# Performance work log

Measured on AMD Instinct MI355X. Metric: run time of the kernel, lower is better.

## Reference

```python
import jax, jax.numpy as jnp
import numpy as np

N_NODES = 50000
N_EDGES = 500000
NUM_FEAT = 128
NUM_CLASSES = 112
HID = 18
HEADS = 8
OUT_DIM = 144  # hidden_dim * heads = 18*8 = 144, also final GAT out_dim
N_GRAPHS = 64
EPS = 1e-5
NEG_SLOPE = 0.2


def setup_inputs() -> dict:
    key = jax.random.key(0)
    ks = jax.random.split(key, 32)
    f32 = jnp.float32
    def rn(k, shape, scale=0.1):
        return jax.random.normal(k, shape, f32) * scale
    x = jax.random.normal(ks[0], (N_NODES, NUM_FEAT), f32)
    edge_index = jax.random.randint(ks[1], (2, N_EDGES), 0, N_NODES)
    batch = jnp.sort(jax.random.randint(ks[2], (N_NODES,), 0, N_GRAPHS))
    D = HID * HEADS  # 144
    params = dict(
        x=x, edge_index=edge_index, batch=batch,
        We=rn(ks[3], (NUM_FEAT, D)), be=jnp.zeros((D,), f32),
        Wg=rn(ks[4], (3, D, D)),
        a_sg=rn(ks[5], (3, HEADS, HID)), a_dg=rn(ks[6], (3, HEADS, HID)),
        bg=jnp.zeros((3, D), f32),
        gam=jnp.ones((3, D), f32), bet=jnp.zeros((3, D), f32),
        W3=rn(ks[7], (D, OUT_DIM)),
        a_s3=rn(ks[8], (1, OUT_DIM)), a_d3=rn(ks[9], (1, OUT_DIM)),
        b3=jnp.zeros((OUT_DIM,), f32),
        gam3=jnp.ones((OUT_DIM,), f32), bet3=jnp.zeros((OUT_DIM,), f32),
        M1=rn(ks[10], (OUT_DIM, 72)), bm1=jnp.zeros((72,), f32),
        gm1=jnp.ones((72,), f32), bb1=jnp.zeros((72,), f32),
        M2=rn(ks[11], (72, 36)), bm2=jnp.zeros((36,), f32),
        gm2=jnp.ones((36,), f32), bb2=jnp.zeros((36,), f32),
        M3=rn(ks[12], (36, NUM_CLASSES)), bm3=jnp.zeros((NUM_CLASSES,), f32),
    )
    return params


def _gat_layer(h, src, dst, W, a_s, a_d, b, heads, out_ch):
    # PyG GATConv: per-head linear, additive attention, segment softmax over dst
    N = h.shape[0]
    hp = (h @ W).reshape(N, heads, out_ch)                 # [N,H,C]
    al_s = (hp * a_s).sum(-1)                              # [N,H]
    al_d = (hp * a_d).sum(-1)                              # [N,H]
    e = jax.nn.leaky_relu(al_s[src] + al_d[dst], NEG_SLOPE)  # [E,H]
    m = jax.ops.segment_max(e, dst, num_segments=N)
    ex = jnp.exp(e - m[dst])
    den = jax.ops.segment_sum(ex, dst, num_segments=N)
    alpha = ex / (den[dst] + 1e-16)                        # [E,H]
    out = jax.ops.segment_sum(hp[src] * alpha[..., None], dst, num_segments=N)
    return out.reshape(N, heads * out_ch) + b


def _bn(x, g, b):
    mu = x.mean(0)
    v = jnp.var(x, axis=0)
    return g * (x - mu) * jax.lax.rsqrt(v + EPS) + b


def reference(x, edge_index, batch, We, be, Wg, a_sg, a_dg, bg, gam, bet,
              W3, a_s3, a_d3, b3, gam3, bet3,
              M1, bm1, gm1, bb1, M2, bm2, gm2, bb2, M3, bm3):
    N = x.shape[0]
    loops = jnp.arange(N)  # GATConv add_self_loops=True
    src = jnp.concatenate([edge_index[0], loops])
    dst = jnp.concatenate([edge_index[1], loops])
    out = x @ We + be
    for i in range(3):
        out = _gat_layer(out, src, dst, Wg[i], a_sg[i], a_dg[i], bg[i], HEADS, HID)
        out = jax.nn.relu(out)
        out = _bn(out, gam[i], bet[i])
    out = _gat_layer(out, src, dst, W3, a_s3, a_d3, b3, 1, OUT_DIM)
    out = jax.nn.relu(out)
    out = _bn(out, gam3, bet3)
    # global mean pool over graphs
    sums = jax.ops.segment_sum(out, batch, num_segments=N_GRAPHS)
    cnt = jax.ops.segment_sum(jnp.ones((N, 1), out.dtype), batch, num_segments=N_GRAPHS)
    g = sums / jnp.maximum(cnt, 1.0)
    # PyG MLP: lin -> batchnorm -> relu (plain last layer)
    h = jax.nn.relu(_bn(g @ M1 + bm1, gm1, bb1))
    h = jax.nn.relu(_bn(h @ M2 + bm2, gm2, bb2))
    return h @ M3 + bm3
```

## Files before the change

### kernel.cpp

```cpp
#include <hip/hip_runtime.h>
#include <cstdint>

#define N_NODESC 50000
#define N_EDGESC 500000
#define E_TOT    550000
#define DIM      144
#define NGRAPH   64
#define EPSV     1e-5f
#define SCAN_NB  ((N_NODESC + 511)/512)

typedef __attribute__((ext_vector_type(8))) short bf16x8;
typedef __attribute__((ext_vector_type(4))) float f32x4;

__device__ __forceinline__ float lrelu(float x){ return x > 0.f ? x : 0.2f*x; }

__device__ __forceinline__ unsigned short f2bf(float f){
  unsigned u = __float_as_uint(f);
  u += 0x7FFF + ((u >> 16) & 1);
  return (unsigned short)(u >> 16);
}
__device__ __forceinline__ float bf2f(unsigned short b){
  return __uint_as_float(((unsigned)b) << 16);
}

__global__ void k_count(const int* __restrict__ ei, int* __restrict__ deg){
  int e = blockIdx.x*blockDim.x + threadIdx.x;
  if (e >= E_TOT) return;
  int d = (e < N_EDGESC) ? ei[N_EDGESC + e] : (e - N_EDGESC);
  atomicAdd(&deg[d], 1);
}

__global__ __launch_bounds__(256) void k_scan1(const int* __restrict__ deg,
    int* __restrict__ scanned, int* __restrict__ bsum){
  __shared__ int ls[256];
  int b = blockIdx.x, t = threadIdx.x;
  int i0 = b*512 + 2*t;
  int e0 = (i0   < N_NODESC) ? deg[i0]   : 0;
  int e1 = (i0+1 < N_NODESC) ? deg[i0+1] : 0;
  int s = e0 + e1;
  ls[t] = s;
  __syncthreads();
  #pragma unroll
  for (int ofs=1; ofs<256; ofs<<=1){
    int v = (t >= ofs) ? ls[t-ofs] : 0;
    __syncthreads();
    ls[t] += v;
    __syncthreads();
  }
  int excl = ls[t] - s;
  if (i0   < N_NODESC) scanned[i0]   = excl;
  if (i0+1 < N_NODESC) scanned[i0+1] = excl + e0;
  if (t == 255) bsum[b] = ls[255];
}

__global__ void k_scan2(int* __restrict__ bsum){
  __shared__ int ls[128];
  int t = threadIdx.x;
  int v = (t < SCAN_NB) ? bsum[t] : 0;
  ls[t] = v;
  __syncthreads();
  #pragma unroll
  for (int ofs=1; ofs<128; ofs<<=1){
    int u = (t >= ofs) ? ls[t-ofs] : 0;
    __syncthreads();
    ls[t] += u;
    __syncthreads();
  }
  if (t < SCAN_NB) bsum[t] = ls[t] - v;
}

__global__ __launch_bounds__(256) void k_scan3(const int* __restrict__ scanned,
    const int* __restrict__ bsum, int* __restrict__ row_ptr, int* __restrict__ cursor){
  int i = blockIdx.x*blockDim.x + threadIdx.x;
  if (i < N_NODESC){
    int v = scanned[i] + bsum[i >> 9];
    row_ptr[i] = v; cursor[i] = v;
  }
  if (i == 0) row_ptr[N_NODESC] = E_TOT;
}

__global__ void k_scatter(const int* __restrict__ ei, int* __restrict__ cursor,
                          int* __restrict__ col){
  int e = blockIdx.x*blockDim.x + threadIdx.x;
  if (e >= E_TOT) return;
  int s, d;
  if (e < N_EDGESC){ s = ei[e]; d = ei[N_EDGESC + e]; } else { s = e - N_EDGESC; d = s; }
  int pos = atomicAdd(&cursor[d], 1);
  col[pos] = s;
}

__global__ void k_cast(const float* __restrict__ x, unsigned short* __restrict__ xb){
  int i = blockIdx.x*blockDim.x + threadIdx.x;
  if (i < N_NODESC*128) xb[i] = f2bf(x[i]);
}

__global__ __launch_bounds__(192) void k_prep_w(
    const float* __restrict__ W, const float* __restrict__ bias_in,
    const float* __restrict__ a_s, const float* __restrict__ a_d,
    const float* __restrict__ bnsum, const float* __restrict__ bngam,
    const float* __restrict__ bnbet,
    unsigned short* __restrict__ Wt, float* __restrict__ bias2,
    int K, int SK, int H){
  __shared__ float red[256];
  int np = blockIdx.x, k = threadIdx.x;
  float sc = 1.f, sh = 0.f;
  if (k < K && bnsum){
    float mu  = bnsum[k] * (1.f/N_NODESC);
    float var = bnsum[K+k] * (1.f/N_NODESC) - mu*mu;
    float inv = rsqrtf(var + EPSV);
    sc = inv * bngam[k];
    sh = bnbet[k] - mu*sc;
  }
  float wcomb = 0.f;
  if (k < K){
    if (np < 144) wcomb = W[(size_t)k*144 + np];
    else if (H > 0){
      int c = np - 144;
      bool iss = c < 8;
      int h = iss ? c : c - 8;
      if (h < H){
        const float* av = iss ? a_s : a_d;
        int C = 144 / H;
        for (int j=0;j<C;++j) wcomb += W[(size_t)k*144 + h*C + j] * av[h*C + j];
      }
    }
  }
  if (k < SK) Wt[(size_t)np*SK + k] = f2bf(wcomb*sc);
  red[k] = (k < K) ? sh*wcomb : 0.f;
  if (k < 64) red[k+192] = 0.f;
  __syncthreads();
  #pragma unroll
  for (int s=128; s>0; s>>=1){
    if (k < s) red[k] += red[k+s];
    __syncthreads();
  }
  if (k == 0){
    float b = red[0];
    if (np < 144 && bias_in) b += bias_in[np];
    bias2[np] = b;
  }
}

template<int NT, int KS, int SK>
__global__ __launch_bounds__(256) void k_mfma_gemm(
    const unsigned short* __restrict__ A,
    const unsigned short* __restrict__ Wt,
    const float* __restrict__ bias2,
    unsigned short* __restrict__ hp,
    float* __restrict__ al_s, float* __restrict__ al_d,
    int KA, int H){
  int t = threadIdx.x;
  int wave = t >> 6, lane = t & 63;
  int c = lane & 15, quad = lane >> 4;
  int m_base = blockIdx.x*64 + wave*16;
  int mA = m_base + c; if (mA > N_NODESC-1) mA = N_NODESC-1;
  f32x4 acc[NT];
  #pragma unroll
  for (int i=0;i<NT;++i) acc[i] = (f32x4){0.f,0.f,0.f,0.f};
  const unsigned short* Arow = A + (size_t)mA*KA + quad*8;
  #pragma unroll
  for (int ks=0; ks<KS; ++ks){
    bf16x8 af = *(const bf16x8*)(Arow + ks*32);
    #pragma unroll
    for (int tt=0; tt<NT; ++tt){
      bf16x8 bfr = *(const bf16x8*)(Wt + (size_t)(tt*16 + c)*SK + ks*32 + quad*8);
      acc[tt] = __builtin_amdgcn_mfma_f32_16x16x32_bf16(af, bfr, acc[tt], 0, 0, 0);
    }
  }
  #pragma unroll
  for (int tt=0; tt<NT; ++tt){
    int n = tt*16 + c;
    float b = bias2[n];
    #pragma unroll
    for (int r=0;r<4;++r){
      int m = m_base + quad*4 + r;
      if (m < N_NODESC){
        float v = acc[tt][r] + b;
        if (n < 144){
          hp[(size_t)m*144 + n] = f2bf(v);
        } else {
          int cc = n - 144;
          if (cc < 8){ if (cc < H) al_s[m*H + cc] = v; }
          else { int h = cc - 8; if (h < H) al_d[m*H + h] = v; }
        }
      }
    }
  }
}

#define EB 8
__global__ __launch_bounds__(256) void k_edge_softmax(
    const float* __restrict__ al_s, const float* __restrict__ al_d,
    const int* __restrict__ row_ptr, const int* __restrict__ col,
    float* __restrict__ esc, int H){
  int idx = blockIdx.x*blockDim.x + threadIdx.x;
  if (idx >= N_NODESC*H) return;
  int n = idx / H, h = idx - n*H;
  int p0 = row_ptr[n], p1 = row_ptr[n+1];
  float ald = al_d[idx];
  float m = -3.4e38f;
  for (int base = p0; base < p1; base += EB){
    int cnt = min(EB, p1 - base);
    int ss[EB];
    #pragma unroll
    for (int i=0;i<EB;++i) if (i<cnt) ss[i] = col[base+i];
    float sc[EB];
    #pragma unroll
    for (int i=0;i<EB;++i) if (i<cnt) sc[i] = lrelu(al_s[ss[i]*H + h] + ald);
    #pragma unroll
    for (int i=0;i<EB;++i) if (i<cnt){
      esc[(size_t)(base+i)*H + h] = sc[i];
      m = fmaxf(m, sc[i]);
    }
  }
  float den = 0.f;
  for (int e = p0; e < p1; ++e) den += __expf(esc[(size_t)e*H + h] - m);
  float inv = 1.f/(den + 1e-16f);
  for (int e = p0; e < p1; ++e)
    esc[(size_t)e*H + h] = __expf(esc[(size_t)e*H + h] - m) * inv;
}

__global__ __launch_bounds__(256) void k_aggregate2(
    const unsigned* __restrict__ hp2, const float* __restrict__ w,
    const int* __restrict__ row_ptr, const int* __restrict__ col,
    const float* __restrict__ bias, unsigned* __restrict__ out,
    int H, int C2){
  int idx = blockIdx.x*blockDim.x + threadIdx.x;
  if (idx >= N_NODESC*72) return;
  int n = idx / 72, cp = idx - n*72;
  int h = cp / C2;
  int p0 = row_ptr[n], p1 = row_ptr[n+1];
  float a0 = 0.f, a1 = 0.f;
  for (int base = p0; base < p1; base += EB){
    int cnt = min(EB, p1 - base);
    int ss[EB]; float ww[EB];
    #pragma unroll
    for (int i=0;i<EB;++i) if (i<cnt){
      ss[i] = col[base+i];
      ww[i] = w[(size_t)(base+i)*H + h];
    }
    unsigned vv[EB];
    #pragma unroll
    for (int i=0;i<EB;++i) if (i<cnt) vv[i] = hp2[(size_t)ss[i]*72 + cp];
    #pragma unroll
    for (int i=0;i<EB;++i) if (i<cnt){
      a0 = fmaf(ww[i], __uint_as_float(vv[i] << 16), a0);
      a1 = fmaf(ww[i], __uint_as_float(vv[i] & 0xFFFF0000u), a1);
    }
  }
  int c0 = 2*cp;
  float r0 = fmaxf(a0 + bias[c0],   0.f);
  float r1 = fmaxf(a1 + bias[c0+1], 0.f);
  out[(size_t)n*72 + cp] = (unsigned)f2bf(r0) | ((unsigned)f2bf(r1) << 16);
}

#define BNS_GRID 512
__global__ __launch_bounds__(256) void k_bnstats1(const uint2* __restrict__ h4,
                                                  float* __restrict__ partials){
  __shared__ float red[252*8];
  int t = threadIdx.x;
  int r = t / 36, c = t - r*36;
  bool active = (t < 252);
  int rows = (N_NODESC + BNS_GRID - 1)/BNS_GRID;
  int n0 = blockIdx.x*rows, n1 = min(N_NODESC, n0+rows);
  float s[4] = {0,0,0,0}, q[4] = {0,0,0,0};
  if (active){
    for (int n = n0 + r; n < n1; n += 7){
      uint2 v = h4[(size_t)n*36 + c];
      float f0 = __uint_as_float(v.x << 16);
      float f1 = __uint_as_float(v.x & 0xFFFF0000u);
      float f2 = __uint_as_float(v.y << 16);
      float f3 = __uint_as_float(v.y & 0xFFFF0000u);
      s[0]+=f0; q[0]+=f0*f0; s[1]+=f1; q[1]+=f1*f1;
      s[2]+=f2; q[2]+=f2*f2; s[3]+=f3; q[3]+=f3*f3;
    }
    #pragma unroll
    for (int j=0;j<4;++j){
      red[(c*7+r)*8 + j]     = s[j];
      red[(c*7+r)*8 + 4 + j] = q[j];
    }
  }
  __syncthreads();
  if (t < 36){
    float ss[4]={0,0,0,0}, qq[4]={0,0,0,0};
    for (int rr=0; rr<7; ++rr){
      #pragma unroll
      for (int j=0;j<4;++j){
        ss[j] += red[(t*7+rr)*8 + j];
        qq[j] += red[(t*7+rr)*8 + 4 + j];
      }
    }
    float* p = partials + (size_t)blockIdx.x*288;
    #pragma unroll
    for (int j=0;j<4;++j){
      p[4*t+j]       = ss[j];
      p[144+4*t+j]   = qq[j];
    }
  }
}

__global__ __launch_bounds__(64) void k_bnstats2(const float* __restrict__ partials,
                                                 float* __restrict__ sums){
  int i = blockIdx.x, t = threadIdx.x;
  float s = 0.f;
  for (int b = t; b < BNS_GRID; b += 64) s += partials[(size_t)b*288 + i];
  #pragma unroll
  for (int o=32; o>0; o>>=1) s += __shfl_xor(s, o, 64);
  if (t == 0) sums[i] = s;
}

__device__ int lbound(const int* a, int n, int v){
  int lo = 0, hi = n;
  while (lo < hi){ int m = (lo+hi) >> 1; if (a[m] < v) lo = m+1; else hi = m; }
  return lo;
}

__global__ __launch_bounds__(128) void k_pool(const unsigned* __restrict__ h2,
    const int* __restrict__ batch, float* __restrict__ sums, int* __restrict__ cnts){
  int g = blockIdx.x & 63, part = blockIdx.x >> 6;
  __shared__ int sb[2];
  if (threadIdx.x == 0){ sb[0] = lbound(batch, N_NODESC, g); sb[1] = lbound(batch, N_NODESC, g+1); }
  __syncthreads();
  int lo = sb[0], hi = sb[1];
  int t = threadIdx.x;
  if (t < 72){
    float a0 = 0.f, a1 = 0.f;
    for (int n = lo + part; n < hi; n += 32){
      unsigned v = h2[(size_t)n*72 + t];
      a0 += __uint_as_float(v << 16);
      a1 += __uint_as_float(v & 0xFFFF0000u);
    }
    atomicAdd(&sums[g*DIM + 2*t],   a0);
    atomicAdd(&sums[g*DIM + 2*t+1], a1);
  }
  if (t == 0 && part == 0) cnts[g] = hi - lo;
}

__global__ __launch_bounds__(64) void k_mlp1(const float* __restrict__ psum,
    const int* __restrict__ cnts,
    const float* __restrict__ bn3, const float* __restrict__ gam3,
    const float* __restrict__ bet3,
    const float* __restrict__ M1, const float* __restrict__ bm1,
    const float* __restrict__ gm1, const float* __restrict__ bb1,
    float* __restrict__ h1){
  __shared__ float sSc[144], sSh[144];
  int t = threadIdx.x, c = blockIdx.x;
  for (int i=t; i<144; i+=64){
    float mu  = bn3[i] * (1.f/N_NODESC);
    float var = bn3[144+i] * (1.f/N_NODESC) - mu*mu;
    float sc  = rsqrtf(var + EPSV) * gam3[i];
    sSc[i] = sc; sSh[i] = bet3[i] - mu*sc;
  }
  __syncthreads();
  float invc = 1.f / (float)max(cnts[t], 1);
  float acc = bm1[c];
  const float* pr = psum + t*144;
  for (int k=0; k<144; ++k){
    float g = fmaf(pr[k]*invc, sSc[k], sSh[k]);
    acc = fmaf(g, M1[k*72 + c], acc);
  }
  float s = acc, q = acc*acc;
  #pragma unroll
  for (int o=32; o>0; o>>=1){ s += __shfl_xor(s, o, 64); q += __shfl_xor(q, o, 64); }
  float mu = s*(1.f/64.f), var = q*(1.f/64.f) - mu*mu;
  float v = (acc - mu)*rsqrtf(var + EPSV)*gm1[c] + bb1[c];
  h1[t*72 + c] = fmaxf(v, 0.f);
}

__global__ __launch_bounds__(64) void k_mlp2(const float* __restrict__ h1,
    const float* __restrict__ M2, const float* __restrict__ bm2,
    const float* __restrict__ gm2, const float* __restrict__ bb2,
    float* __restrict__ h2){
  int t = threadIdx.x, c = blockIdx.x;
  float acc = bm2[c];
  const float* pr = h1 + t*72;
  for (int k=0; k<72; ++k) acc = fmaf(pr[k], M2[k*36 + c], acc);
  float s = acc, q = acc*acc;
  #pragma unroll
  for (int o=32; o>0; o>>=1){ s += __shfl_xor(s, o, 64); q += __shfl_xor(q, o, 64); }
  float mu = s*(1.f/64.f), var = q*(1.f/64.f) - mu*mu;
  float v = (acc - mu)*rsqrtf(var + EPSV)*gm2[c] + bb2[c];
  h2[t*36 + c] = fmaxf(v, 0.f);
}

__global__ __launch_bounds__(64) void k_mlp3(const float* __restrict__ h2,
    const float* __restrict__ M3, const float* __restrict__ bm3,
    float* __restrict__ out){
  int t = threadIdx.x, c = blockIdx.x;
  float acc = bm3[c];
  const float* pr = h2 + t*36;
  for (int k=0; k<36; ++k) acc = fmaf(pr[k], M3[k*112 + c], acc);
  out[t*112 + c] = acc;
}

extern "C" void kernel_launch(void* const* d_in, const int* in_sizes, int n_in,
                              void* d_out, int out_size, void* d_ws, size_t ws_size,
                              hipStream_t stream){
  const float* x    = (const float*)d_in[0];
  const int*   ei   = (const int*)d_in[1];
  const int*   batch= (const int*)d_in[2];
  const float* We   = (const float*)d_in[3];
  const float* be   = (const float*)d_in[4];
  const float* Wg   = (const float*)d_in[5];
  const float* a_sg = (const float*)d_in[6];
  const float* a_dg = (const float*)d_in[7];
  const float* bg   = (const float*)d_in[8];
  const float* gam  = (const float*)d_in[9];
  const float* bet  = (const float*)d_in[10];
  const float* W3   = (const float*)d_in[11];
  const float* a_s3 = (const float*)d_in[12];
  const float* a_d3 = (const float*)d_in[13];
  const float* b3   = (const float*)d_in[14];
  const float* gam3 = (const float*)d_in[15];
  const float* bet3 = (const float*)d_in[16];
  const float* M1   = (const float*)d_in[17];
  const float* bm1  = (const float*)d_in[18];
  const float* gm1  = (const float*)d_in[19];
  const float* bb1  = (const float*)d_in[20];
  const float* M2   = (const float*)d_in[21];
  const float* bm2  = (const float*)d_in[22];
  const float* gm2  = (const float*)d_in[23];
  const float* bb2  = (const float*)d_in[24];
  const float* M3   = (const float*)d_in[25];
  const float* bm3  = (const float*)d_in[26];
  float* out = (float*)d_out;

  char* ws = (char*)d_ws;
  size_t off = 0;
  auto alloc = [&](size_t bytes)->char*{
    char* p = ws + off; off += (bytes + 255) & ~(size_t)255; return p;
  };
  unsigned short* hAb = (unsigned short*)alloc((size_t)N_NODESC*DIM*2);
  unsigned short* hp  = (unsigned short*)alloc((size_t)N_NODESC*DIM*2);
  unsigned short* xb  = (unsigned short*)alloc((size_t)N_NODESC*128*2);
  float* al_s   = (float*)alloc((size_t)N_NODESC*8*4);
  float* al_d   = (float*)alloc((size_t)N_NODESC*8*4);
  float* esc    = (float*)alloc((size_t)E_TOT*8*4);
  int* row_ptr  = (int*)alloc((size_t)(N_NODESC+1)*4);
  int* deg      = (int*)alloc((size_t)N_NODESC*4);
  int* cursor   = (int*)alloc((size_t)N_NODESC*4);
  int* scanned  = (int*)alloc((size_t)N_NODESC*4);
  int* bsum     = (int*)alloc((size_t)SCAN_NB*4);
  int* col      = (int*)alloc((size_t)E_TOT*4);
  float* bns4   = (float*)alloc(4*2*DIM*4);
  float* partials = (float*)alloc((size_t)BNS_GRID*288*4);
  float* psum   = (float*)alloc((size_t)NGRAPH*DIM*4);
  int* pcnt     = (int*)alloc(NGRAPH*4);
  float* h1buf  = (float*)alloc((size_t)NGRAPH*72*4);
  float* h2buf  = (float*)alloc((size_t)NGRAPH*36*4);
  unsigned short* Wt = (unsigned short*)alloc((size_t)160*168*2);
  float* bias2  = (float*)alloc(160*4);
  (void)ws_size; (void)n_in; (void)in_sizes; (void)out_size;

  const int GEMM_GRID = (N_NODESC + 63)/64;

  hipMemsetAsync(deg, 0, (size_t)N_NODESC*4, stream);
  k_count<<<(E_TOT+255)/256, 256, 0, stream>>>(ei, deg);
  k_scan1<<<SCAN_NB, 256, 0, stream>>>(deg, scanned, bsum);
  k_scan2<<<1, 128, 0, stream>>>(bsum);
  k_scan3<<<(N_NODESC+255)/256, 256, 0, stream>>>(scanned, bsum, row_ptr, cursor);
  k_scatter<<<(E_TOT+255)/256, 256, 0, stream>>>(ei, cursor, col);

  k_cast<<<(N_NODESC*128+255)/256, 256, 0, stream>>>(x, xb);
  k_prep_w<<<144, 192, 0, stream>>>(We, be, nullptr, nullptr,
                                    nullptr, nullptr, nullptr, Wt, bias2, 128, 136, 0);
  k_mfma_gemm<9,4,136><<<GEMM_GRID, 256, 0, stream>>>(
      xb, Wt, bias2, hAb, nullptr, nullptr, 128, 0);

  for (int L=0; L<4; ++L){
    const float* W  = (L<3) ? (Wg  + (size_t)L*DIM*DIM) : W3;
    const float* as = (L<3) ? (a_sg + (size_t)L*8*18)   : a_s3;
    const float* ad = (L<3) ? (a_dg + (size_t)L*8*18)   : a_d3;
    const float* bb = (L<3) ? (bg  + L*DIM) : b3;
    int H = (L<3) ? 8 : 1;
    int C = (L<3) ? 18 : 144;
    const float* bnp = (L==0) ? nullptr : bns4 + (size_t)(L-1)*2*DIM;
    const float* gmp = (L==0) ? nullptr : gam + (size_t)(L-1)*DIM;
    const float* btp = (L==0) ? nullptr : bet + (size_t)(L-1)*DIM;
    k_prep_w<<<160, 192, 0, stream>>>(W, nullptr, as, ad,
                                      bnp, gmp, btp, Wt, bias2, 144, 168, H);
    k_mfma_gemm<10,5,168><<<GEMM_GRID, 256, 0, stream>>>(
        hAb, Wt, bias2, hp, al_s, al_d, 144, H);
    k_edge_softmax<<<(N_NODESC*H+255)/256, 256, 0, stream>>>(
        al_s, al_d, row_ptr, col, esc, H);
    k_aggregate2<<<(N_NODESC*72+255)/256, 256, 0, stream>>>(
        (const unsigned*)hp, esc, row_ptr, col, bb, (unsigned*)hAb, H, C/2);
    k_bnstats1<<<BNS_GRID, 256, 0, stream>>>((const uint2*)hAb, partials);
    k_bnstats2<<<288, 64, 0, stream>>>(partials, bns4 + (size_t)L*2*DIM);
  }

  hipMemsetAsync(psum, 0, (size_t)NGRAPH*DIM*4, stream);
  k_pool<<<NGRAPH*32, 128, 0, stream>>>((const unsigned*)hAb, batch, psum, pcnt);
  k_mlp1<<<72, 64, 0, stream>>>(psum, pcnt, bns4 + 3*2*DIM, gam3, bet3,
                                M1, bm1, gm1, bb1, h1buf);
  k_mlp2<<<36, 64, 0, stream>>>(h1buf, M2, bm2, gm2, bb2, h2buf);
  k_mlp3<<<112, 64, 0, stream>>>(h2buf, M3, bm3, out);
}
```

Baseline: 674.8 us.

## Block hp by channel group and make attention weights head-major for aggregation

The GEMM now writes hp in a channel-group-blocked layout (8 groups of 9 bf16 pairs per node), and edge softmax stores scores head-major. The aggregation kernel is regridded so each block handles one channel group for 28 nodes, which shrinks the gathered working set per block to a 36-byte slice per node. The aim is better L2 locality for random neighbour gathers. The costs are scattered GEMM stores, 4 idle threads per block, and 36-byte row gathers that are less coalesced.

```diff
diff --git a/kernel.cpp b/kernel.cpp
--- a/kernel.cpp
+++ b/kernel.cpp
@@ -148,7 +148,7 @@
     const float* __restrict__ bias2,
     unsigned short* __restrict__ hp,
     float* __restrict__ al_s, float* __restrict__ al_d,
-    int KA, int H){
+    int KA, int H, int blocked){
   int t = threadIdx.x;
   int wave = t >> 6, lane = t & 63;
   int c = lane & 15, quad = lane >> 4;
@@ -171,13 +171,19 @@
   for (int tt=0; tt<NT; ++tt){
     int n = tt*16 + c;
     float b = bias2[n];
+    int p = n >> 1, cgx = p/9, jj = p - 9*cgx, lo = n & 1;
     #pragma unroll
     for (int r=0;r<4;++r){
       int m = m_base + quad*4 + r;
       if (m < N_NODESC){
         float v = acc[tt][r] + b;
         if (n < 144){
-          hp[(size_t)m*144 + n] = f2bf(v);
+          if (blocked){
+            size_t idx = (size_t)cgx*9*N_NODESC + (size_t)m*9 + jj;
+            hp[2*idx + lo] = f2bf(v);
+          } else {
+            hp[(size_t)m*144 + n] = f2bf(v);
+          }
         } else {
           int cc = n - 144;
           if (cc < 8){ if (cc < H) al_s[m*H + cc] = v; }
@@ -198,6 +204,7 @@
   int n = idx / H, h = idx - n*H;
   int p0 = row_ptr[n], p1 = row_ptr[n+1];
   float ald = al_d[idx];
+  float* er = esc + (size_t)h*E_TOT;
   float m = -3.4e38f;
   for (int base = p0; base < p1; base += EB){
     int cnt = min(EB, p1 - base);
@@ -209,26 +216,35 @@
     for (int i=0;i<EB;++i) if (i<cnt) sc[i] = lrelu(al_s[ss[i]*H + h] + ald);
     #pragma unroll
     for (int i=0;i<EB;++i) if (i<cnt){
-      esc[(size_t)(base+i)*H + h] = sc[i];
+      er[base+i] = sc[i];
       m = fmaxf(m, sc[i]);
     }
   }
   float den = 0.f;
-  for (int e = p0; e < p1; ++e) den += __expf(esc[(size_t)e*H + h] - m);
+  for (int e = p0; e < p1; ++e) den += __expf(er[e] - m);
   float inv = 1.f/(den + 1e-16f);
   for (int e = p0; e < p1; ++e)
-    esc[(size_t)e*H + h] = __expf(esc[(size_t)e*H + h] - m) * inv;
-}
-
+    er[e] = __expf(er[e] - m) * inv;
+}
+
+#define AGG_NPB 28
 __global__ __launch_bounds__(256) void k_aggregate2(
-    const unsigned* __restrict__ hp2, const float* __restrict__ w,
+    const unsigned* __restrict__ hpb, const float* __restrict__ w,
     const int* __restrict__ row_ptr, const int* __restrict__ col,
     const float* __restrict__ bias, unsigned* __restrict__ out,
     int H, int C2){
-  int idx = blockIdx.x*blockDim.x + threadIdx.x;
-  if (idx >= N_NODESC*72) return;
-  int n = idx / 72, cp = idx - n*72;
+  int cg = blockIdx.x & 7;
+  int nb = blockIdx.x >> 3;
+  int t = threadIdx.x;
+  if (t >= 252) return;
+  int tn = t / 9;
+  int n = nb*AGG_NPB + tn;
+  if (n >= N_NODESC) return;
+  int j = t - tn*9;
+  int cp = cg*9 + j;
   int h = cp / C2;
+  const unsigned* hpc = hpb + (size_t)cg*9*N_NODESC;
+  const float* wh = w + (size_t)h*E_TOT;
   int p0 = row_ptr[n], p1 = row_ptr[n+1];
   float a0 = 0.f, a1 = 0.f;
   for (int base = p0; base < p1; base += EB){
@@ -237,11 +253,11 @@
     #pragma unroll
     for (int i=0;i<EB;++i) if (i<cnt){
       ss[i] = col[base+i];
-      ww[i] = w[(size_t)(base+i)*H + h];
+      ww[i] = wh[base+i];
     }
     unsigned vv[EB];
     #pragma unroll
-    for (int i=0;i<EB;++i) if (i<cnt) vv[i] = hp2[(size_t)ss[i]*72 + cp];
+    for (int i=0;i<EB;++i) if (i<cnt) vv[i] = hpc[(size_t)ss[i]*9 + j];
     #pragma unroll
     for (int i=0;i<EB;++i) if (i<cnt){
       a0 = fmaf(ww[i], __uint_as_float(vv[i] << 16), a0);
@@ -453,6 +469,7 @@
   (void)ws_size; (void)n_in; (void)in_sizes; (void)out_size;
 
   const int GEMM_GRID = (N_NODESC + 63)/64;
+  const int AGG_GRID = 8 * ((N_NODESC + AGG_NPB - 1)/AGG_NPB);
 
   hipMemsetAsync(deg, 0, (size_t)N_NODESC*4, stream);
   k_count<<<(E_TOT+255)/256, 256, 0, stream>>>(ei, deg);
@@ -465,7 +482,7 @@
   k_prep_w<<<144, 192, 0, stream>>>(We, be, nullptr, nullptr,
                                     nullptr, nullptr, nullptr, Wt, bias2, 128, 136, 0);
   k_mfma_gemm<9,4,136><<<GEMM_GRID, 256, 0, stream>>>(
-      xb, Wt, bias2, hAb, nullptr, nullptr, 128, 0);
+      xb, Wt, bias2, hAb, nullptr, nullptr, 128, 0, 0);
 
   for (int L=0; L<4; ++L){
     const float* W  = (L<3) ? (Wg  + (size_t)L*DIM*DIM) : W3;
@@ -480,10 +497,10 @@
     k_prep_w<<<160, 192, 0, stream>>>(W, nullptr, as, ad,
                                       bnp, gmp, btp, Wt, bias2, 144, 168, H);
     k_mfma_gemm<10,5,168><<<GEMM_GRID, 256, 0, stream>>>(
-        hAb, Wt, bias2, hp, al_s, al_d, 144, H);
+        hAb, Wt, bias2, hp, al_s, al_d, 144, H, 1);
     k_edge_softmax<<<(N_NODESC*H+255)/256, 256, 0, stream>>>(
         al_s, al_d, row_ptr, col, esc, H);
-    k_aggregate2<<<(N_NODESC*72+255)/256, 256, 0, stream>>>(
+    k_aggregate2<<<AGG_GRID, 256, 0, stream>>>(
         (const unsigned*)hp, esc, row_ptr, col, bb, (unsigned*)hAb, H, C/2);
     k_bnstats1<<<BNS_GRID, 256, 0, stream>>>((const uint2*)hAb, partials);
     k_bnstats2<<<288, 64, 0, stream>>>(partials, bns4 + (size_t)L*2*DIM);
```

Result: slower. 856.3 us (+26.9%).
